# Performance work log

Hardware: AMD Instinct MI355X
Metric: run time of the kernel (lower is better)

## Reference

```python
import jax, jax.numpy as jnp
import numpy as np

D_MODEL = 1024
N_HEADS = 16
HEAD_DIM = D_MODEL // N_HEADS


def setup_inputs() -> dict:
    key = jax.random.key(0)
    ks = jax.random.split(key, 5)
    s = 0.02  # small init scale to keep softmax numerics reasonable
    x = jax.random.normal(ks[0], (4, 2048, D_MODEL), dtype=jnp.float32)
    w_qkv = jax.random.normal(ks[1], (D_MODEL, 3 * D_MODEL), dtype=jnp.float32) * s
    b_qkv = jnp.zeros((3 * D_MODEL,), dtype=jnp.float32)
    w_proj = jax.random.normal(ks[2], (D_MODEL, D_MODEL), dtype=jnp.float32) * s
    b_proj = jnp.zeros((D_MODEL,), dtype=jnp.float32)
    return {"x": x, "w_qkv": w_qkv, "b_qkv": b_qkv, "w_proj": w_proj, "b_proj": b_proj}


def reference(x, w_qkv, b_qkv, w_proj, b_proj):
    B, T, C = x.shape
    scale = 1.0 / np.sqrt(HEAD_DIM)
    qkv = x @ w_qkv + b_qkv                               # [B,T,3C]
    qkv = qkv.reshape(B, T, 3, N_HEADS, HEAD_DIM)
    q = qkv[:, :, 0].transpose(0, 2, 1, 3)               # [B,H,T,D]
    k = qkv[:, :, 1].transpose(0, 2, 1, 3)
    v = qkv[:, :, 2].transpose(0, 2, 1, 3)
    att = jnp.einsum('bhqd,bhkd->bhqk', q, k) * scale    # [B,H,T,T]
    causal = jnp.tril(jnp.ones((T, T), dtype=bool))
    att = jnp.where(causal, att, -jnp.inf)
    att = jax.nn.softmax(att, axis=-1)
    y = jnp.einsum('bhqk,bhkd->bhqd', att, v)            # [B,H,T,D]
    y = y.transpose(0, 2, 1, 3).reshape(B, T, C)
    y = y @ w_proj + b_proj
    return y
```

## Files before the change

### kernel.cpp

```cpp
#include <hip/hip_runtime.h>
#include <stdint.h>

#define BATCH 4
#define SEQ 2048
#define DMODEL 1024
#define NHEADS 16
#define HDIM 64
#define MROWS (BATCH * SEQ)

typedef float floatx4 __attribute__((ext_vector_type(4)));
typedef __bf16 bf16x8 __attribute__((ext_vector_type(8)));
typedef __bf16 bf16x4 __attribute__((ext_vector_type(4)));
typedef short short8 __attribute__((ext_vector_type(8)));

__device__ __forceinline__ unsigned short f32_to_bf16(float f) {
    union { float f; unsigned int u; } c; c.f = f;
    unsigned int u = c.u;
    unsigned int r = (u + 0x7FFFu + ((u >> 16) & 1u)) >> 16;
    return (unsigned short)r;
}

__device__ __forceinline__ void async_ld16(const void* g, void* l) {
    __builtin_amdgcn_global_load_lds(
        (const __attribute__((address_space(1))) unsigned int*)g,
        (__attribute__((address_space(3))) unsigned int*)l, 16, 0, 0);
}

__global__ __launch_bounds__(256) void conv_f32_bf16(
    const float* __restrict__ in, unsigned short* __restrict__ out, int n4) {
    int i = blockIdx.x * 256 + threadIdx.x;
    if (i < n4) {
        float4 v = ((const float4*)in)[i];
        ushort4 o;
        o.x = f32_to_bf16(v.x); o.y = f32_to_bf16(v.y);
        o.z = f32_to_bf16(v.z); o.w = f32_to_bf16(v.w);
        ((ushort4*)out)[i] = o;
    }
}

__global__ __launch_bounds__(256) void transp_conv(
    const float* __restrict__ in, unsigned short* __restrict__ out, int K, int N) {
    __shared__ float tile[32][33];
    int bx = blockIdx.x * 32;
    int by = blockIdx.y * 32;
    int tx = threadIdx.x, ty = threadIdx.y;
#pragma unroll
    for (int i = 0; i < 4; ++i)
        tile[ty + i * 8][tx] = in[(size_t)(by + ty + i * 8) * N + bx + tx];
    __syncthreads();
#pragma unroll
    for (int i = 0; i < 4; ++i)
        out[(size_t)(bx + ty + i * 8) * K + by + tx] = f32_to_bf16(tile[tx][ty + i * 8]);
}

__global__ __launch_bounds__(256) void transp_bf16_head(
    const unsigned short* __restrict__ in, unsigned short* __restrict__ out) {
    __shared__ unsigned short tile[32][33];
    const unsigned short* src = in + (size_t)blockIdx.z * SEQ * HDIM;
    unsigned short* dst = out + (size_t)blockIdx.z * SEQ * HDIM;
    int bx = blockIdx.x * 32;
    int by = blockIdx.y * 32;
    int tx = threadIdx.x, ty = threadIdx.y;
#pragma unroll
    for (int i = 0; i < 4; ++i)
        tile[ty + i * 8][tx] = src[(size_t)(by + ty + i * 8) * HDIM + bx + tx];
    __syncthreads();
#pragma unroll
    for (int i = 0; i < 4; ++i) {
        int keyg = by + tx;
        int col2 = (keyg & ~63) | (((keyg & 15) << 2) | ((keyg >> 4) & 3));
        dst[(size_t)(bx + ty + i * 8) * SEQ + col2] = tile[tx][ty + i * 8];
    }
}

template <int EPI>
__global__ __launch_bounds__(256, 3) void gemm_bt(
    const unsigned short* __restrict__ A, const unsigned short* __restrict__ Bt,
    const float* __restrict__ bias, float* __restrict__ Cout,
    unsigned short* __restrict__ Qo, unsigned short* __restrict__ Ko,
    unsigned short* __restrict__ Vo, int M, int N, int K) {
    __shared__ __align__(16) unsigned short As[3][128 * 32];
    __shared__ __align__(16) unsigned short Bs[3][128 * 32];
    const int tid = threadIdx.x;
    const int lane = tid & 63;
    const int w = tid >> 6;
    const int wm = w & 1, wn = w >> 1;
    const int quad = lane >> 4, l16 = lane & 15;

    const int nbx = gridDim.x;
    const int nwg = nbx * gridDim.y;
    const int lin = blockIdx.y * nbx + blockIdx.x;
    const int swz = (lin & 7) * (nwg >> 3) + (lin >> 3);
    const int m0 = (swz / nbx) * 128;
    const int n0 = (swz % nbx) * 128;
    const int fsw = (l16 >> 1) & 3;

    const int idx0 = tid, idx1 = tid + 256;
    const int row0 = idx0 >> 2, row1 = idx1 >> 2;
    const int cg0 = (idx0 & 3) ^ ((row0 >> 1) & 3);
    const int cg1 = (idx1 & 3) ^ ((row1 >> 1) & 3);
    const unsigned short* Ar0 = &A[(size_t)(m0 + row0) * K + cg0 * 8];
    const unsigned short* Ar1 = &A[(size_t)(m0 + row1) * K + cg1 * 8];
    const unsigned short* Br0 = &Bt[(size_t)(n0 + row0) * K + cg0 * 8];
    const unsigned short* Br1 = &Bt[(size_t)(n0 + row1) * K + cg1 * 8];

    floatx4 acc[4][4];
#pragma unroll
    for (int mt = 0; mt < 4; ++mt)
#pragma unroll
        for (int nt = 0; nt < 4; ++nt) acc[mt][nt] = (floatx4){0.f, 0.f, 0.f, 0.f};

    async_ld16(Ar0, &As[0][idx0 * 8]);
    async_ld16(Br0, &Bs[0][idx0 * 8]);
    async_ld16(Ar1, &As[0][idx1 * 8]);
    async_ld16(Br1, &Bs[0][idx1 * 8]);
    async_ld16(Ar0 + 32, &As[1][idx0 * 8]);
    async_ld16(Br0 + 32, &Bs[1][idx0 * 8]);
    async_ld16(Ar1 + 32, &As[1][idx1 * 8]);
    async_ld16(Br1 + 32, &Bs[1][idx1 * 8]);

    const int nk = K >> 5;
    int bcur = 0, bpre = 2;
    for (int kt = 0; kt < nk; ++kt) {
        if (kt + 2 < nk)
            asm volatile("s_waitcnt vmcnt(4)" ::: "memory");
        else
            asm volatile("s_waitcnt vmcnt(0)" ::: "memory");
        __builtin_amdgcn_s_barrier();
        asm volatile("" ::: "memory");

        if (kt + 2 < nk) {
            const int ko = (kt + 2) << 5;
            async_ld16(Ar0 + ko, &As[bpre][idx0 * 8]);
            async_ld16(Br0 + ko, &Bs[bpre][idx0 * 8]);
            async_ld16(Ar1 + ko, &As[bpre][idx1 * 8]);
            async_ld16(Br1 + ko, &Bs[bpre][idx1 * 8]);
        }

        bf16x8 aF[4], bF[4];
#pragma unroll
        for (int mt = 0; mt < 4; ++mt)
            aF[mt] = *(const bf16x8*)&As[bcur][(wm * 64 + mt * 16 + l16) * 32 + (quad ^ fsw) * 8];
#pragma unroll
        for (int nt = 0; nt < 4; ++nt)
            bF[nt] = *(const bf16x8*)&Bs[bcur][(wn * 64 + nt * 16 + l16) * 32 + (quad ^ fsw) * 8];
#pragma unroll
        for (int mt = 0; mt < 4; ++mt)
#pragma unroll
            for (int nt = 0; nt < 4; ++nt)
                acc[mt][nt] = __builtin_amdgcn_mfma_f32_16x16x32_bf16(
                    aF[mt], bF[nt], acc[mt][nt], 0, 0, 0);

        bcur = (bcur == 2) ? 0 : bcur + 1;
        bpre = (bpre == 2) ? 0 : bpre + 1;
    }

#pragma unroll
    for (int mt = 0; mt < 4; ++mt)
#pragma unroll
        for (int nt = 0; nt < 4; ++nt)
#pragma unroll
            for (int r = 0; r < 4; ++r) {
                int m = m0 + wm * 64 + mt * 16 + quad * 4 + r;
                int n = n0 + wn * 64 + nt * 16 + l16;
                float v = acc[mt][nt][r] + bias[n];
                if (EPI == 1) {
                    Cout[(size_t)m * N + n] = v;
                } else {
                    int sel = n >> 10, c = n & 1023;
                    int head = c >> 6, d = c & 63;
                    int bb = m >> 11, t = m & 2047;
                    unsigned short* dst = sel == 0 ? Qo : (sel == 1 ? Ko : Vo);
                    dst[((((size_t)bb * NHEADS + head) * SEQ + t) << 6) + d] = f32_to_bf16(v);
                }
            }
}

__global__ __launch_bounds__(256, 2) void attn_kernel(
    const unsigned short* __restrict__ Qg, const unsigned short* __restrict__ Kg,
    const unsigned short* __restrict__ Vtg, unsigned short* __restrict__ Yatt) {
    __shared__ __align__(16) unsigned short Kb2[3][4096];
    __shared__ __align__(16) unsigned short Vb2[3][4096];
    __shared__ __align__(16) unsigned short Ps[4][2048];

    const int tid = threadIdx.x;
    const int lane = tid & 63;
    const int w = tid >> 6;
    const int quad = lane >> 4, l16 = lane & 15;
    const int bh = blockIdx.x;
    const int by = blockIdx.y;
    const int sA = by * 4 + w;
    const size_t base = (size_t)bh * SEQ * HDIM;
    const int bIdx = bh >> 4, h = bh & 15;
    unsigned short* Pw = &Ps[w][0];
    const float csc = 0.18033688f;

    const int lrow = lane >> 3;
    const int lch = (lane & 7) ^ lrow;

    short8 osv = {0x3F80, 0x3F80, 0x3F80, 0x3F80, 0x3F80, 0x3F80, 0x3F80, 0x3F80};
    bf16x8 ones = __builtin_bit_cast(bf16x8, osv);

    const unsigned short* Ktg = Kg + base;
    const unsigned short* Vtg_t = Vtg + base;
    const int i0 = w * 2, i1 = w * 2 + 1;
    const int kof0 = (i0 * 8 + lrow) * 64 + lch * 8;
    const int kof1 = (i1 * 8 + lrow) * 64 + lch * 8;
    const size_t vof0 = (size_t)(i0 * 8 + lrow) * SEQ + lch * 8;
    const size_t vof1 = (size_t)(i1 * 8 + lrow) * SEQ + lch * 8;
    const int ld0 = i0 * 512 + lane * 8;
    const int ld1 = i1 * 512 + lane * 8;

    for (int half = 0; half < 2; ++half) {
        const int rowb = (half == 0 ? sA : 63 - sA) * 32;
        const int kmaxB = (half == 0) ? (2 * by + 2) : (32 - 2 * by);

        bf16x8 qf[2][2];
#pragma unroll
        for (int mt = 0; mt < 2; ++mt)
#pragma unroll
            for (int kk = 0; kk < 2; ++kk)
                qf[mt][kk] = *(const bf16x8*)&Qg[base + (size_t)(rowb + mt * 16 + l16) * 64 +
                                                 kk * 32 + quad * 8];

        floatx4 lsum[2];
        floatx4 o[2][4];
#pragma unroll
        for (int mt = 0; mt < 2; ++mt) {
            lsum[mt] = (floatx4){0.f, 0.f, 0.f, 0.f};
#pragma unroll
            for (int nt = 0; nt < 4; ++nt) o[mt][nt] = (floatx4){0.f, 0.f, 0.f, 0.f};
        }

        async_ld16(Ktg + kof0, &Kb2[0][ld0]);
        async_ld16(Vtg_t + vof0, &Vb2[0][ld0]);
        async_ld16(Ktg + kof1, &Kb2[0][ld1]);
        async_ld16(Vtg_t + vof1, &Vb2[0][ld1]);
        async_ld16(Ktg + 64 * HDIM + kof0, &Kb2[1][ld0]);
        async_ld16(Vtg_t + 64 + vof0, &Vb2[1][ld0]);
        async_ld16(Ktg + 64 * HDIM + kof1, &Kb2[1][ld1]);
        async_ld16(Vtg_t + 64 + vof1, &Vb2[1][ld1]);

        int bcur = 0, bpre = 2;
        for (int kb = 0; kb < kmaxB; ++kb) {
            if (kb + 2 < kmaxB)
                asm volatile("s_waitcnt vmcnt(4)" ::: "memory");
            else
                asm volatile("s_waitcnt vmcnt(0)" ::: "memory");
            __builtin_amdgcn_s_barrier();
            asm volatile("" ::: "memory");

            if (kb + 2 < kmaxB) {
                const unsigned short* Kt2 = Ktg + (size_t)(kb + 2) * 64 * HDIM;
                const unsigned short* Vt2 = Vtg_t + (kb + 2) * 64;
                async_ld16(Kt2 + kof0, &Kb2[bpre][ld0]);
                async_ld16(Vt2 + vof0, &Vb2[bpre][ld0]);
                async_ld16(Kt2 + kof1, &Kb2[bpre][ld1]);
                async_ld16(Vt2 + vof1, &Vb2[bpre][ld1]);
            }

            floatx4 s[2][4];
#pragma unroll
            for (int mt = 0; mt < 2; ++mt)
#pragma unroll
                for (int nt = 0; nt < 4; ++nt) s[mt][nt] = (floatx4){0.f, 0.f, 0.f, 0.f};
#pragma unroll
            for (int kk = 0; kk < 2; ++kk) {
                bf16x8 kf[4];
#pragma unroll
                for (int nt = 0; nt < 4; ++nt)
                    kf[nt] = *(const bf16x8*)&Kb2[bcur][(nt * 16 + l16) * 64 +
                                                        ((kk * 4 + quad) ^ (l16 & 7)) * 8];
#pragma unroll
                for (int nt = 0; nt < 4; ++nt)
#pragma unroll
                    for (int mt = 0; mt < 2; ++mt)
                        s[mt][nt] = __builtin_amdgcn_mfma_f32_16x16x32_bf16(
                            qf[mt][kk], kf[nt], s[mt][nt], 0, 0, 0);
            }

            if ((kb * 64 + 63) > rowb) {
#pragma unroll
                for (int mt = 0; mt < 2; ++mt)
#pragma unroll
                    for (int nt = 0; nt < 4; ++nt)
#pragma unroll
                        for (int r = 0; r < 4; ++r) {
                            int key = kb * 64 + nt * 16 + l16;
                            int qrow = rowb + mt * 16 + quad * 4 + r;
                            if (key > qrow) s[mt][nt][r] = -INFINITY;
                        }
            }

#pragma unroll
            for (int mt = 0; mt < 2; ++mt)
#pragma unroll
                for (int nt = 0; nt < 4; ++nt)
#pragma unroll
                    for (int r = 0; r < 4; ++r)
                        s[mt][nt][r] = __builtin_amdgcn_exp2f(s[mt][nt][r] * csc);

#pragma unroll
            for (int mt = 0; mt < 2; ++mt)
#pragma unroll
                for (int r = 0; r < 4; ++r) {
                    int prow = mt * 16 + quad * 4 + r;
                    int unit = l16 ^ (prow & 14);
                    floatx4 t = {s[mt][0][r], s[mt][1][r], s[mt][2][r], s[mt][3][r]};
                    bf16x4 pv = __builtin_convertvector(t, bf16x4);
                    *(bf16x4*)&Pw[prow * 64 + unit * 4] = pv;
                }

#pragma unroll
            for (int kk = 0; kk < 2; ++kk) {
                bf16x8 af[2];
#pragma unroll
                for (int mt = 0; mt < 2; ++mt) {
                    int prow = mt * 16 + l16;
                    int u2 = (kk * 8 + quad * 2) ^ (l16 & 14);
                    af[mt] = *(const bf16x8*)&Pw[prow * 64 + u2 * 4];
                }
#pragma unroll
                for (int nt = 0; nt < 4; ++nt) {
                    bf16x8 vf = *(const bf16x8*)&Vb2[bcur][(nt * 16 + l16) * 64 +
                                                           ((kk * 4 + quad) ^ (l16 & 7)) * 8];
#pragma unroll
                    for (int mt = 0; mt < 2; ++mt)
                        o[mt][nt] = __builtin_amdgcn_mfma_f32_16x16x32_bf16(
                            af[mt], vf, o[mt][nt], 0, 0, 0);
                }
#pragma unroll
                for (int mt = 0; mt < 2; ++mt)
                    lsum[mt] = __builtin_amdgcn_mfma_f32_16x16x32_bf16(
                        af[mt], ones, lsum[mt], 0, 0, 0);
            }

            bcur = (bcur == 2) ? 0 : bcur + 1;
            bpre = (bpre == 2) ? 0 : bpre + 1;
        }

        __syncthreads();

#pragma unroll
        for (int mt = 0; mt < 2; ++mt)
#pragma unroll
            for (int r = 0; r < 4; ++r) {
                float inv = 1.0f / lsum[mt][r];
                int qrow = rowb + mt * 16 + quad * 4 + r;
#pragma unroll
                for (int nt = 0; nt < 4; ++nt)
                    Yatt[((size_t)(bIdx * SEQ + qrow) << 10) + h * 64 + nt * 16 + l16] =
                        f32_to_bf16(o[mt][nt][r] * inv);
            }
    }
}

extern "C" void kernel_launch(void* const* d_in, const int* in_sizes, int n_in,
                              void* d_out, int out_size, void* d_ws, size_t ws_size,
                              hipStream_t stream) {
    const float* x = (const float*)d_in[0];
    const float* w_qkv = (const float*)d_in[1];
    const float* b_qkv = (const float*)d_in[2];
    const float* w_proj = (const float*)d_in[3];
    const float* b_proj = (const float*)d_in[4];
    float* out = (float*)d_out;

    char* ws = (char*)d_ws;
    unsigned short* xb     = (unsigned short*)(ws);
    unsigned short* wqkvT  = (unsigned short*)(ws + 16777216);
    unsigned short* wprojT = (unsigned short*)(ws + 23068672);
    unsigned short* Qb     = (unsigned short*)(ws + 25165824);
    unsigned short* Kb     = (unsigned short*)(ws + 41943040);
    unsigned short* Vb     = (unsigned short*)(ws + 58720256);
    unsigned short* Yatt   = (unsigned short*)(ws + 75497472);
    unsigned short* Vt     = (unsigned short*)(ws + 92274688);

    conv_f32_bf16<<<8192, 256, 0, stream>>>(x, xb, (MROWS * DMODEL) / 4);
    transp_conv<<<dim3(96, 32), dim3(32, 8), 0, stream>>>(w_qkv, wqkvT, DMODEL, 3 * DMODEL);
    transp_conv<<<dim3(32, 32), dim3(32, 8), 0, stream>>>(w_proj, wprojT, DMODEL, DMODEL);
    gemm_bt<0><<<dim3(24, 64), 256, 0, stream>>>(xb, wqkvT, b_qkv, nullptr, Qb, Kb, Vb,
                                                 MROWS, 3 * DMODEL, DMODEL);
    transp_bf16_head<<<dim3(2, 64, BATCH * NHEADS), dim3(32, 8), 0, stream>>>(Vb, Vt);
    attn_kernel<<<dim3(64, 8), 256, 0, stream>>>(Qb, Kb, Vt, Yatt);
    gemm_bt<1><<<dim3(8, 64), 256, 0, stream>>>(Yatt, wprojT, b_proj, out, nullptr, nullptr,
                                                nullptr, MROWS, DMODEL, DMODEL);
}
```

Measured before the change: 253.3 us.

## Process both causal query strips per K/V block and fuse prep kernels

The attention kernel now loads each K/V block once and applies it to both the early and late query strips of a warp, instead of looping over the two strips separately and streaming K/V twice. This halves the K/V global-to-LDS traffic and the number of pipeline prologues and barriers per block, at the cost of holding two sets of Q fragments and accumulators (more registers). The three input conversion and transpose kernels are also merged into a single launch to cut launch overhead.

After: 248.8 us. No clear change (-1.8%).

```diff
diff --git a/kernel.cpp b/kernel.cpp
--- a/kernel.cpp
+++ b/kernel.cpp
@@ -26,31 +26,33 @@
         (__attribute__((address_space(3))) unsigned int*)l, 16, 0, 0);
 }
 
-__global__ __launch_bounds__(256) void conv_f32_bf16(
-    const float* __restrict__ in, unsigned short* __restrict__ out, int n4) {
-    int i = blockIdx.x * 256 + threadIdx.x;
-    if (i < n4) {
-        float4 v = ((const float4*)in)[i];
+__global__ __launch_bounds__(256) void prep_kernel(
+    const float* __restrict__ x, unsigned short* __restrict__ xb,
+    const float* __restrict__ w_qkv, unsigned short* __restrict__ wqkvT,
+    const float* __restrict__ w_proj, unsigned short* __restrict__ wprojT) {
+    const int gx = blockIdx.x, gy = blockIdx.y;
+    const int tx = threadIdx.x, ty = threadIdx.y;
+    if (gx < 256) {
+        int i = (gx * 32 + gy) * 256 + ty * 32 + tx;
+        float4 v = ((const float4*)x)[i];
         ushort4 o;
         o.x = f32_to_bf16(v.x); o.y = f32_to_bf16(v.y);
         o.z = f32_to_bf16(v.z); o.w = f32_to_bf16(v.w);
-        ((ushort4*)out)[i] = o;
-    }
-}
-
-__global__ __launch_bounds__(256) void transp_conv(
-    const float* __restrict__ in, unsigned short* __restrict__ out, int K, int N) {
+        ((ushort4*)xb)[i] = o;
+        return;
+    }
     __shared__ float tile[32][33];
-    int bx = blockIdx.x * 32;
-    int by = blockIdx.y * 32;
-    int tx = threadIdx.x, ty = threadIdx.y;
+    const float* in; unsigned short* out; int N, bx;
+    if (gx < 352) { in = w_qkv; out = wqkvT; N = 3072; bx = (gx - 256) * 32; }
+    else          { in = w_proj; out = wprojT; N = 1024; bx = (gx - 352) * 32; }
+    const int by = gy * 32;
 #pragma unroll
     for (int i = 0; i < 4; ++i)
         tile[ty + i * 8][tx] = in[(size_t)(by + ty + i * 8) * N + bx + tx];
     __syncthreads();
 #pragma unroll
     for (int i = 0; i < 4; ++i)
-        out[(size_t)(bx + ty + i * 8) * K + by + tx] = f32_to_bf16(tile[tx][ty + i * 8]);
+        out[(size_t)(bx + ty + i * 8) * DMODEL + by + tx] = f32_to_bf16(tile[tx][ty + i * 8]);
 }
 
 __global__ __launch_bounds__(256) void transp_bf16_head(
@@ -176,6 +178,88 @@
             }
 }
 
+__device__ __forceinline__ void strip_body(
+    int kb, int rowb, int quad, int l16,
+    const bf16x8 (&qf)[2][2], const unsigned short* Kb, const unsigned short* Vb,
+    unsigned short* Pw, bf16x8 ones, float csc,
+    floatx4 (&o)[2][4], floatx4 (&lsum)[2]) {
+    floatx4 s[2][4];
+#pragma unroll
+    for (int mt = 0; mt < 2; ++mt)
+#pragma unroll
+        for (int nt = 0; nt < 4; ++nt) s[mt][nt] = (floatx4){0.f, 0.f, 0.f, 0.f};
+#pragma unroll
+    for (int kk = 0; kk < 2; ++kk) {
+        bf16x8 kf[4];
+#pragma unroll
+        for (int nt = 0; nt < 4; ++nt)
+            kf[nt] = *(const bf16x8*)&Kb[(nt * 16 + l16) * 64 +
+                                         ((kk * 4 + quad) ^ (l16 & 7)) * 8];
+#pragma unroll
+        for (int nt = 0; nt < 4; ++nt)
+#pragma unroll
+            for (int mt = 0; mt < 2; ++mt)
+                s[mt][nt] = __builtin_amdgcn_mfma_f32_16x16x32_bf16(
+                    qf[mt][kk], kf[nt], s[mt][nt], 0, 0, 0);
+    }
+
+    if ((kb * 64 + 63) > rowb) {
+#pragma unroll
+        for (int mt = 0; mt < 2; ++mt)
+#pragma unroll
+            for (int nt = 0; nt < 4; ++nt)
+#pragma unroll
+                for (int r = 0; r < 4; ++r) {
+                    int key = kb * 64 + nt * 16 + l16;
+                    int qrow = rowb + mt * 16 + quad * 4 + r;
+                    if (key > qrow) s[mt][nt][r] = -INFINITY;
+                }
+    }
+
+#pragma unroll
+    for (int mt = 0; mt < 2; ++mt)
+#pragma unroll
+        for (int nt = 0; nt < 4; ++nt)
+#pragma unroll
+            for (int r = 0; r < 4; ++r)
+                s[mt][nt][r] = __builtin_amdgcn_exp2f(s[mt][nt][r] * csc);
+
+#pragma unroll
+    for (int mt = 0; mt < 2; ++mt)
+#pragma unroll
+        for (int r = 0; r < 4; ++r) {
+            int prow = mt * 16 + quad * 4 + r;
+            int unit = l16 ^ (prow & 14);
+            floatx4 t = {s[mt][0][r], s[mt][1][r], s[mt][2][r], s[mt][3][r]};
+            bf16x4 pv = __builtin_convertvector(t, bf16x4);
+            *(bf16x4*)&Pw[prow * 64 + unit * 4] = pv;
+        }
+
+#pragma unroll
+    for (int kk = 0; kk < 2; ++kk) {
+        bf16x8 af[2];
+#pragma unroll
+        for (int mt = 0; mt < 2; ++mt) {
+            int prow = mt * 16 + l16;
+            int u2 = (kk * 8 + quad * 2) ^ (l16 & 14);
+            af[mt] = *(const bf16x8*)&Pw[prow * 64 + u2 * 4];
+        }
+#pragma unroll
+        for (int nt = 0; nt < 4; ++nt) {
+            bf16x8 vf = *(const bf16x8*)&Vb[(nt * 16 + l16) * 64 +
+                                            ((kk * 4 + quad) ^ (l16 & 7)) * 8];
+#pragma unroll
+            for (int mt = 0; mt < 2; ++mt)
+                o[mt][nt] = __builtin_amdgcn_mfma_f32_16x16x32_bf16(
+                    af[mt], vf, o[mt][nt], 0, 0, 0);
+        }
+#pragma unroll
+        for (int mt = 0; mt < 2; ++mt)
+            lsum[mt] = __builtin_amdgcn_mfma_f32_16x16x32_bf16(
+                af[mt], ones, lsum[mt], 0, 0, 0);
+    }
+}
+
 __global__ __launch_bounds__(256, 2) void attn_kernel(
     const unsigned short* __restrict__ Qg, const unsigned short* __restrict__ Kg,
     const unsigned short* __restrict__ Vtg, unsigned short* __restrict__ Yatt) {
@@ -201,6 +285,13 @@
     short8 osv = {0x3F80, 0x3F80, 0x3F80, 0x3F80, 0x3F80, 0x3F80, 0x3F80, 0x3F80};
     bf16x8 ones = __builtin_bit_cast(bf16x8, osv);
 
+    const int rowbA = sA * 32;
+    const int rowbB = (63 - sA) * 32;
+    const int tA = 2 * by + 2, tB = 32 - 2 * by;
+    const int kmaxB = tA > tB ? tA : tB;
+    const int lastA = sA >> 1;
+    const int lastB = (2047 - 32 * sA) >> 6;
+
     const unsigned short* Ktg = Kg + base;
     const unsigned short* Vtg_t = Vtg + base;
     const int i0 = w * 2, i1 = w * 2 + 1;
@@ -211,148 +302,85 @@
     const int ld0 = i0 * 512 + lane * 8;
     const int ld1 = i1 * 512 + lane * 8;
 
-    for (int half = 0; half < 2; ++half) {
-        const int rowb = (half == 0 ? sA : 63 - sA) * 32;
-        const int kmaxB = (half == 0) ? (2 * by + 2) : (32 - 2 * by);
-
-        bf16x8 qf[2][2];
-#pragma unroll
-        for (int mt = 0; mt < 2; ++mt)
-#pragma unroll
-            for (int kk = 0; kk < 2; ++kk)
-                qf[mt][kk] = *(const bf16x8*)&Qg[base + (size_t)(rowb + mt * 16 + l16) * 64 +
-                                                 kk * 32 + quad * 8];
-
-        floatx4 lsum[2];
-        floatx4 o[2][4];
-#pragma unroll
-        for (int mt = 0; mt < 2; ++mt) {
-            lsum[mt] = (floatx4){0.f, 0.f, 0.f, 0.f};
-#pragma unroll
-            for (int nt = 0; nt < 4; ++nt) o[mt][nt] = (floatx4){0.f, 0.f, 0.f, 0.f};
-        }
-
-        async_ld16(Ktg + kof0, &Kb2[0][ld0]);
-        async_ld16(Vtg_t + vof0, &Vb2[0][ld0]);
-        async_ld16(Ktg + kof1, &Kb2[0][ld1]);
-        async_ld16(Vtg_t + vof1, &Vb2[0][ld1]);
-        async_ld16(Ktg + 64 * HDIM + kof0, &Kb2[1][ld0]);
-        async_ld16(Vtg_t + 64 + vof0, &Vb2[1][ld0]);
-        async_ld16(Ktg + 64 * HDIM + kof1, &Kb2[1][ld1]);
-        async_ld16(Vtg_t + 64 + vof1, &Vb2[1][ld1]);
-
-        int bcur = 0, bpre = 2;
-        for (int kb = 0; kb < kmaxB; ++kb) {
-            if (kb + 2 < kmaxB)
-                asm volatile("s_waitcnt vmcnt(4)" ::: "memory");
-            else
-                asm volatile("s_waitcnt vmcnt(0)" ::: "memory");
-            __builtin_amdgcn_s_barrier();
-            asm volatile("" ::: "memory");
-
-            if (kb + 2 < kmaxB) {
-                const unsigned short* Kt2 = Ktg + (size_t)(kb + 2) * 64 * HDIM;
-                const unsigned short* Vt2 = Vtg_t + (kb + 2) * 64;
-                async_ld16(Kt2 + kof0, &Kb2[bpre][ld0]);
-                async_ld16(Vt2 + vof0, &Vb2[bpre][ld0]);
-                async_ld16(Kt2 + kof1, &Kb2[bpre][ld1]);
-                async_ld16(Vt2 + vof1, &Vb2[bpre][ld1]);
+    bf16x8 qfA[2][2], qfB[2][2];
+#pragma unroll
+    for (int mt = 0; mt < 2; ++mt)
+#pragma unroll
+        for (int kk = 0; kk < 2; ++kk) {
+            qfA[mt][kk] = *(const bf16x8*)&Qg[base + (size_t)(rowbA + mt * 16 + l16) * 64 +
+                                              kk * 32 + quad * 8];
+            qfB[mt][kk] = *(const bf16x8*)&Qg[base + (size_t)(rowbB + mt * 16 + l16) * 64 +
+                                              kk * 32 + quad * 8];
+        }
+    asm volatile("" ::: "memory");
+
+    floatx4 lsumA[2], lsumB[2];
+    floatx4 oA[2][4], oB[2][4];
+#pragma unroll
+    for (int mt = 0; mt < 2; ++mt) {
+        lsumA[mt] = (floatx4){0.f, 0.f, 0.f, 0.f};
+        lsumB[mt] = (floatx4){0.f, 0.f, 0.f, 0.f};
+#pragma unroll
+        for (int nt = 0; nt < 4; ++nt) {
+            oA[mt][nt] = (floatx4){0.f, 0.f, 0.f, 0.f};
+            oB[mt][nt] = (floatx4){0.f, 0.f, 0.f, 0.f};
+        }
+    }
+
+    async_ld16(Ktg + kof0, &Kb2[0][ld0]);
+    async_ld16(Vtg_t + vof0, &Vb2[0][ld0]);
+    async_ld16(Ktg + kof1, &Kb2[0][ld1]);
+    async_ld16(Vtg_t + vof1, &Vb2[0][ld1]);
+    async_ld16(Ktg + 64 * HDIM + kof0, &Kb2[1][ld0]);
+    async_ld16(Vtg_t + 64 + vof0, &Vb2[1][ld0]);
+    async_ld16(Ktg + 64 * HDIM + kof1, &Kb2[1][ld1]);
+    async_ld16(Vtg_t + 64 + vof1, &Vb2[1][ld1]);
+
+    int bcur = 0, bpre = 2;
+    for (int kb = 0; kb < kmaxB; ++kb) {
+        if (kb + 2 < kmaxB)
+            asm volatile("s_waitcnt vmcnt(4)" ::: "memory");
+        else
+            asm volatile("s_waitcnt vmcnt(0)" ::: "memory");
+        __builtin_amdgcn_s_barrier();
+        asm volatile("" ::: "memory");
+
+        if (kb + 2 < kmaxB) {
+            const unsigned short* Kt2 = Ktg + (size_t)(kb + 2) * 64 * HDIM;
+            const unsigned short* Vt2 = Vtg_t + (kb + 2) * 64;
+            async_ld16(Kt2 + kof0, &Kb2[bpre][ld0]);
+            async_ld16(Vt2 + vof0, &Vb2[bpre][ld0]);
+            async_ld16(Kt2 + kof1, &Kb2[bpre][ld1]);
+            async_ld16(Vt2 + vof1, &Vb2[bpre][ld1]);
+        }
+
+        if (kb <= lastA)
+            strip_body(kb, rowbA, quad, l16, qfA, &Kb2[bcur][0], &Vb2[bcur][0],
+                       Pw, ones, csc, oA, lsumA);
+        if (kb <= lastB)
+            strip_body(kb, rowbB, quad, l16, qfB, &Kb2[bcur][0], &Vb2[bcur][0],
+                       Pw, ones, csc, oB, lsumB);
+
+        bcur = (bcur == 2) ? 0 : bcur + 1;
+        bpre = (bpre == 2) ? 0 : bpre + 1;
+    }
+
+#pragma unroll
+    for (int mt = 0; mt < 2; ++mt)
+#pragma unroll
+        for (int r = 0; r < 4; ++r) {
+            float invA = 1.0f / lsumA[mt][r];
+            float invB = 1.0f / lsumB[mt][r];
+            int qrowA = rowbA + mt * 16 + quad * 4 + r;
+            int qrowB = rowbB + mt * 16 + quad * 4 + r;
+#pragma unroll
+            for (int nt = 0; nt < 4; ++nt) {
+                Yatt[((size_t)(bIdx * SEQ + qrowA) << 10) + h * 64 + nt * 16 + l16] =
+                    f32_to_bf16(oA[mt][nt][r] * invA);
+                Yatt[((size_t)(bIdx * SEQ + qrowB) << 10) + h * 64 + nt * 16 + l16] =
+                    f32_to_bf16(oB[mt][nt][r] * invB);
             }
-
-            floatx4 s[2][4];
-#pragma unroll
-            for (int mt = 0; mt < 2; ++mt)
-#pragma unroll
-                for (int nt = 0; nt < 4; ++nt) s[mt][nt] = (floatx4){0.f, 0.f, 0.f, 0.f};
-#pragma unroll
-            for (int kk = 0; kk < 2; ++kk) {
-                bf16x8 kf[4];
-#pragma unroll
-                for (int nt = 0; nt < 4; ++nt)
-                    kf[nt] = *(const bf16x8*)&Kb2[bcur][(nt * 16 + l16) * 64 +
-                                                        ((kk * 4 + quad) ^ (l16 & 7)) * 8];
-#pragma unroll
-                for (int nt = 0; nt < 4; ++nt)
-#pragma unroll
-                    for (int mt = 0; mt < 2; ++mt)
-                        s[mt][nt] = __builtin_amdgcn_mfma_f32_16x16x32_bf16(
-                            qf[mt][kk], kf[nt], s[mt][nt], 0, 0, 0);
-            }
-
-            if ((kb * 64 + 63) > rowb) {
-#pragma unroll
-                for (int mt = 0; mt < 2; ++mt)
-#pragma unroll
-                    for (int nt = 0; nt < 4; ++nt)
-#pragma unroll
-                        for (int r = 0; r < 4; ++r) {
-                            int key = kb * 64 + nt * 16 + l16;
-                            int qrow = rowb + mt * 16 + quad * 4 + r;
-                            if (key > qrow) s[mt][nt][r] = -INFINITY;
-                        }
-            }
-
-#pragma unroll
-            for (int mt = 0; mt < 2; ++mt)
-#pragma unroll
-                for (int nt = 0; nt < 4; ++nt)
-#pragma unroll
-                    for (int r = 0; r < 4; ++r)
-                        s[mt][nt][r] = __builtin_amdgcn_exp2f(s[mt][nt][r] * csc);
-
-#pragma unroll
-            for (int mt = 0; mt < 2; ++mt)
-#pragma unroll
-                for (int r = 0; r < 4; ++r) {
-                    int prow = mt * 16 + quad * 4 + r;
-                    int unit = l16 ^ (prow & 14);
-                    floatx4 t = {s[mt][0][r], s[mt][1][r], s[mt][2][r], s[mt][3][r]};
-                    bf16x4 pv = __builtin_convertvector(t, bf16x4);
-                    *(bf16x4*)&Pw[prow * 64 + unit * 4] = pv;
-                }
-
-#pragma unroll
-            for (int kk = 0; kk < 2; ++kk) {
-                bf16x8 af[2];
-#pragma unroll
-                for (int mt = 0; mt < 2; ++mt) {
-                    int prow = mt * 16 + l16;
-                    int u2 = (kk * 8 + quad * 2) ^ (l16 & 14);
-                    af[mt] = *(const bf16x8*)&Pw[prow * 64 + u2 * 4];
-                }
-#pragma unroll
-                for (int nt = 0; nt < 4; ++nt) {
-                    bf16x8 vf = *(const bf16x8*)&Vb2[bcur][(nt * 16 + l16) * 64 +
-                                                           ((kk * 4 + quad) ^ (l16 & 7)) * 8];
-#pragma unroll
-                    for (int mt = 0; mt < 2; ++mt)
-                        o[mt][nt] = __builtin_amdgcn_mfma_f32_16x16x32_bf16(
-                            af[mt], vf, o[mt][nt], 0, 0, 0);
-                }
-#pragma unroll
-                for (int mt = 0; mt < 2; ++mt)
-                    lsum[mt] = __builtin_amdgcn_mfma_f32_16x16x32_bf16(
-                        af[mt], ones, lsum[mt], 0, 0, 0);
-            }
-
-            bcur = (bcur == 2) ? 0 : bcur + 1;
-            bpre = (bpre == 2) ? 0 : bpre + 1;
-        }
-
-        __syncthreads();
-
-#pragma unroll
-        for (int mt = 0; mt < 2; ++mt)
-#pragma unroll
-            for (int r = 0; r < 4; ++r) {
-                float inv = 1.0f / lsum[mt][r];
-                int qrow = rowb + mt * 16 + quad * 4 + r;
-#pragma unroll
-                for (int nt = 0; nt < 4; ++nt)
-                    Yatt[((size_t)(bIdx * SEQ + qrow) << 10) + h * 64 + nt * 16 + l16] =
-                        f32_to_bf16(o[mt][nt][r] * inv);
-            }
-    }
+        }
 }
 
 extern "C" void kernel_launch(void* const* d_in, const int* in_sizes, int n_in,
@@ -375,9 +403,8 @@
     unsigned short* Yatt   = (unsigned short*)(ws + 75497472);
     unsigned short* Vt     = (unsigned short*)(ws + 92274688);
 
-    conv_f32_bf16<<<8192, 256, 0, stream>>>(x, xb, (MROWS * DMODEL) / 4);
-    transp_conv<<<dim3(96, 32), dim3(32, 8), 0, stream>>>(w_qkv, wqkvT, DMODEL, 3 * DMODEL);
-    transp_conv<<<dim3(32, 32), dim3(32, 8), 0, stream>>>(w_proj, wprojT, DMODEL, DMODEL);
+    prep_kernel<<<dim3(384, 32), dim3(32, 8), 0, stream>>>(x, xb, w_qkv, wqkvT,
+                                                           w_proj, wprojT);
     gemm_bt<0><<<dim3(24, 64), 256, 0, stream>>>(xb, wqkvT, b_qkv, nullptr, Qb, Kb, Vb,
                                                  MROWS, 3 * DMODEL, DMODEL);
     transp_bf16_head<<<dim3(2, 64, BATCH * NHEADS), dim3(32, 8), 0, stream>>>(Vb, Vt);
```
